# Kernel optimization log

Measured on AMD Instinct MI355X. Metric: run time of the kernel, lower is better.

Reference implementation:

```python
import jax, jax.numpy as jnp
import numpy as np
import math

NDIM = 1
K = 7            # kernel_size ** ndim
C = 256          # channels
G = C            # depthwise -> groups == channels
GC = 1           # group_channels
HID = 32
OMEGA = 30.0
OFFSET_SCALE = 2.0
MIN_SIGMA, MAX_SIGMA = 0.05, 0.5
INIT_SIGMA = 0.3


def setup_inputs() -> dict:
    key = jax.random.key(0)
    ks = jax.random.split(key, 24)
    B, L = 4, 4096
    init_raw = math.log(math.exp(INIT_SIGMA) - 1.0)
    nrm = jax.random.normal
    d = {
        "x": nrm(ks[0], (B, L, C), jnp.float32),
        "raw_sigma": jnp.full((NDIM,), init_raw, jnp.float32),
        # input/output projections (stored as (in, out): y = x @ W + b)
        "w_in": nrm(ks[1], (C, C)) * (1.0 / np.sqrt(C)),
        "b_in": nrm(ks[2], (C,)) * 0.01,
        "w_out": nrm(ks[3], (C, C)) * (1.0 / np.sqrt(C)),
        "b_out": nrm(ks[4], (C,)) * 0.01,
        # dw_conv: depthwise 3-tap conv (OIH with I=1), then 1x1 conv (in,out)
        "dw1_w": nrm(ks[5], (C, 1, 3)) * (1.0 / np.sqrt(3)),
        "dw1_b": nrm(ks[6], (C,)) * 0.01,
        "dw2_w": nrm(ks[7], (C, C)) * (1.0 / np.sqrt(C)),
        "dw2_b": nrm(ks[8], (C,)) * 0.01,
        # offset / mask nets (zero-init in original; small random to exercise sampling)
        "w_off": nrm(ks[9], (C, G * K * NDIM)) * 0.01,
        "b_off": nrm(ks[10], (G * K * NDIM,)) * 0.01,
        "w_mask": nrm(ks[11], (C, G * K)) * 0.01,
        "b_mask": nrm(ks[12], (G * K,)) * 0.01,
        # kernel net: Linear(1,32), SiLU, Linear(32,32), SiLU, Linear(32,32), SiLU, Linear(32, G*GC)
        "k0_w": nrm(ks[13], (NDIM, HID)) * 1.0,
        "k0_b": nrm(ks[14], (HID,)) * 0.01,
        "k1_w": nrm(ks[15], (HID, HID)) * (1.0 / np.sqrt(HID)),
        "k1_b": nrm(ks[16], (HID,)) * 0.01,
        "k2_w": nrm(ks[17], (HID, HID)) * (1.0 / np.sqrt(HID)),
        "k2_b": nrm(ks[18], (HID,)) * 0.01,
        "k3_w": nrm(ks[19], (HID, G * GC)) * (1.0 / np.sqrt(HID)),
        "k3_b": nrm(ks[20], (G * GC,)) * 0.01,
    }
    return d


def _forward(x, raw_sigma, w_in, b_in, w_out, b_out, dw1_w, dw1_b, dw2_w, dw2_b,
             w_off, b_off, w_mask, b_mask, k0_w, k0_b, k1_w, k1_b, k2_w, k2_b, k3_w, k3_b):
    B, L, Cc = x.shape
    grid = jnp.linspace(-0.5, 0.5, K)[:, None]                       # (K, NDIM)
    ref_off = (jnp.arange(K, dtype=x.dtype) - K // 2)[:, None]        # (K, NDIM)

    sigma = jnp.clip(jax.nn.softplus(raw_sigma), MIN_SIGMA, MAX_SIGMA)

    x_proj = x @ w_in + b_in                                          # (B, L, C)

    # dw_conv: depthwise conv3 -> SiLU -> conv1x1, on (B, C, L)
    xc = jnp.transpose(x, (0, 2, 1))
    h = jax.lax.conv_general_dilated(xc, dw1_w, (1,), ((1, 1),),
                                     dimension_numbers=("NCH", "OIH", "NCH"),
                                     feature_group_count=Cc)
    h = jax.nn.silu(h + dw1_b[None, :, None])
    h = jnp.einsum("bcl,cd->bdl", h, dw2_w) + dw2_b[None, :, None]
    x_dw = jnp.transpose(h, (0, 2, 1))                                # (B, L, C)

    # Gaussian envelope over kernel taps
    d2 = (grid / jnp.clip(sigma, 1e-6, None)[None, :]) ** 2
    env = jnp.exp(-0.5 * d2.sum(-1))                                  # (K,)
    env = env / jnp.maximum(env.sum(), 1e-8)

    # implicit kernel weights from kernel net (SIREN-style input scaling)
    kh = jax.nn.silu(grid * OMEGA @ k0_w + k0_b)
    kh = jax.nn.silu(kh @ k1_w + k1_b)
    kh = jax.nn.silu(kh @ k2_w + k2_b)
    kernel_weights = kh @ k3_w + k3_b                                 # (K, G*GC)

    offsets = jnp.tanh(x_dw @ w_off + b_off).reshape(B, L, G, K, NDIM) * OFFSET_SCALE
    pos = jnp.arange(L, dtype=x.dtype).reshape(1, L, 1, 1, 1)
    abs_pos = pos + ref_off.reshape(1, 1, 1, K, NDIM) + offsets       # (B,L,G,K,1)

    # ---- bilinear (linear, ndim=1) sampling with gather ----
    p = jnp.clip(abs_pos[..., 0], 0.0, L - 1)                         # (B,L,G,K)
    pf = p.astype(jnp.int32)
    pc = jnp.minimum(pf + 1, L - 1)
    wc = (p - pf.astype(p.dtype))[..., None]                          # (B,L,G,K,1)
    wf = 1.0 - wc

    x_t = x_proj.reshape(B, L, G, GC).transpose(0, 2, 1, 3)           # (B,G,L,GC)

    def gather(idx):  # idx (B,L,G,K) int -> (B,L,G,K,GC)
        it = idx.transpose(0, 2, 1, 3).reshape(B, G, L * K, 1)
        g = jnp.take_along_axis(x_t, it, axis=2)
        return g.reshape(B, G, L, K, GC).transpose(0, 2, 1, 3, 4)

    sampled = gather(pf) * wf + gather(pc) * wc                       # (B,L,G,K,GC)

    kw = kernel_weights.reshape(G, GC, K).transpose(0, 2, 1)          # (G,K,GC) (raw reshape as in original)
    sampled = sampled * kw[None, None]

    raw_mask = (x_dw @ w_mask + b_mask).reshape(B, L, G, K) * env.reshape(1, 1, 1, K)
    attn = jax.nn.softmax(raw_mask, axis=-1)

    out = (sampled * attn[..., None]).sum(3).reshape(B, L, Cc)
    out = out @ w_out + b_out

    offset_reg = (offsets ** 2).mean()
    entropy = -(attn * jnp.log(attn + 1e-8)).sum(-1).mean()
    return out, offset_reg, -entropy


def reference(x, raw_sigma, w_in, b_in, w_out, b_out, dw1_w, dw1_b, dw2_w, dw2_b,
              w_off, b_off, w_mask, b_mask, k0_w, k0_b, k1_w, k1_b, k2_w, k2_b, k3_w, k3_b):
    return _forward(x, raw_sigma, w_in, b_in, w_out, b_out, dw1_w, dw1_b, dw2_w, dw2_b,
                    w_off, b_off, w_mask, b_mask, k0_w, k0_b, k1_w, k1_b, k2_w, k2_b, k3_w, k3_b)
```

## Files before the change

kernel.cpp:

```cpp
#include <hip/hip_runtime.h>
#include <hip/hip_bf16.h>
#include <hip/hip_fp16.h>
#include <math.h>

#define BB   4
#define LL   4096
#define CCH  256
#define KK   7
#define HIDN 32
#define MTOT (BB * LL)
#define NOFF (CCH * KK)
#define NP   4096
#define NBLK ((NP / 128) * (MTOT / 128))

#define LOG2E  1.4426950408889634f
#define NLOG2E2 (-2.8853900817779268f)
#define LN2    0.6931471805599453f

typedef __attribute__((ext_vector_type(8))) short short8;
typedef __attribute__((ext_vector_type(4))) short short4v;
typedef __attribute__((ext_vector_type(4))) float f32x4;
typedef __attribute__((ext_vector_type(2))) __fp16 fp16x2;
typedef __attribute__((address_space(1))) void gvoid_t;
typedef __attribute__((address_space(3))) void svoid_t;

__device__ __forceinline__ float siluf(float v) { return v / (1.0f + expf(-v)); }
__device__ __forceinline__ float bf2f(ushort u) { unsigned x = (unsigned)u << 16; return __uint_as_float(x); }
__device__ __forceinline__ float h2f(ushort u) { __half_raw hr; hr.x = u; return __half2float(__half(hr)); }
__device__ __forceinline__ unsigned pkh(float a, float b) {
    union { fp16x2 h; unsigned u; } cv;
    cv.h = __builtin_amdgcn_cvt_pkrtz(a, b);
    return cv.u;
}

__global__ __launch_bounds__(256) void precompute_kernel(
    const float* __restrict__ raw_sigma,
    const float* __restrict__ k0w, const float* __restrict__ k0b,
    const float* __restrict__ k1w, const float* __restrict__ k1b,
    const float* __restrict__ k2w, const float* __restrict__ k2b,
    const float* __restrict__ k3w, const float* __restrict__ k3b,
    const float* __restrict__ b_off, const float* __restrict__ b_mask,
    float* __restrict__ kws2, float* __restrict__ bcomb,
    float* __restrict__ env)
{
    __shared__ float h0[KK][HIDN];
    __shared__ float h1[KK][HIDN];
    __shared__ float h2[KK][HIDN];
    __shared__ float flatw[NOFF];
    __shared__ float envs[KK];
    int t = threadIdx.x;
    if (t < KK * HIDN) {
        int k = t / HIDN, j = t % HIDN;
        float gk = -0.5f + (float)k * (1.0f / 6.0f);
        float v = gk * 30.0f * k0w[j] + k0b[j];
        h0[k][j] = siluf(v);
    }
    __syncthreads();
    if (t < KK * HIDN) {
        int k = t / HIDN, j = t % HIDN;
        float s = k1b[j];
        #pragma unroll
        for (int i = 0; i < HIDN; ++i) s += h0[k][i] * k1w[i * HIDN + j];
        h1[k][j] = siluf(s);
    }
    __syncthreads();
    if (t < KK * HIDN) {
        int k = t / HIDN, j = t % HIDN;
        float s = k2b[j];
        #pragma unroll
        for (int i = 0; i < HIDN; ++i) s += h1[k][i] * k2w[i * HIDN + j];
        h2[k][j] = siluf(s);
    }
    __syncthreads();
    for (int k = 0; k < KK; ++k) {
        float s = k3b[t];
        #pragma unroll
        for (int i = 0; i < HIDN; ++i) s += h2[k][i] * k3w[i * CCH + t];
        flatw[k * CCH + t] = s;
    }
    if (t == 0) {
        float sp = log1pf(expf(raw_sigma[0]));
        sp = fminf(fmaxf(sp, 0.05f), 0.5f);
        float sg = fmaxf(sp, 1e-6f);
        float ev[KK]; float ssum = 0.0f;
        for (int k = 0; k < KK; ++k) {
            float gk = -0.5f + (float)k * (1.0f / 6.0f);
            float d = gk / sg;
            ev[k] = expf(-0.5f * d * d);
            ssum += ev[k];
        }
        ssum = fmaxf(ssum, 1e-8f);
        for (int k = 0; k < KK; ++k) { env[k] = ev[k] / ssum; envs[k] = ev[k] / ssum; }
    }
    __syncthreads();
    #pragma unroll
    for (int k = 0; k < KK; ++k) kws2[t * 8 + k] = flatw[t * KK + k];
    kws2[t * 8 + 7] = 0.0f;
    #pragma unroll
    for (int k = 0; k < KK; ++k) {
        bcomb[t * 16 + k]     = b_off[t * KK + k] * NLOG2E2;
        bcomb[t * 16 + 8 + k] = b_mask[t * KK + k] * envs[k] * LOG2E;
    }
    bcomb[t * 16 + 7]  = 0.0f;
    bcomb[t * 16 + 15] = 0.0f;
}

__global__ __launch_bounds__(256) void prep_kernel(
    const float* __restrict__ w_in, const float* __restrict__ dw2_w,
    const float* __restrict__ w_out, const float* __restrict__ w_off,
    const float* __restrict__ w_mask, const float* __restrict__ env,
    __hip_bfloat16* __restrict__ wtin, __hip_bfloat16* __restrict__ wtdw2,
    __hip_bfloat16* __restrict__ wtout, __hip_bfloat16* __restrict__ wtcomb)
{
    const int task = blockIdx.y;
    const int tid = threadIdx.x;
    if (task == 5) {
        if (blockIdx.x >= 64) return;
        unsigned u = blockIdx.x * 256 + tid;
        unsigned row_sel = u >> 5, chunk = u & 31;
        unsigned g = row_sel >> 1, which = row_sel & 1;
        unsigned row = g * 16 + 7 + which * 8;
        short8 z = {};
        *(short8*)((ushort*)wtcomb + (size_t)row * 256 + chunk * 8) = z;
        return;
    }
    const float* src; __hip_bfloat16* dst; int N; int mode = 0;
    switch (task) {
        case 0: src = w_in;  dst = wtin;  N = 256;  break;
        case 1: src = dw2_w; dst = wtdw2; N = 256;  break;
        case 2: src = w_out; dst = wtout; N = 256;  break;
        case 3: src = w_off;  dst = wtcomb; N = NOFF; mode = 1; break;
        default: src = w_mask; dst = wtcomb; N = NOFF; mode = 2; break;
    }
    int ntiles = 4 * (N / 64);
    if (blockIdx.x >= (unsigned)ntiles) return;
    int tk = (blockIdx.x & 3) * 64;
    int tn = (blockIdx.x >> 2) * 64;
    __shared__ float t[64][65];
    #pragma unroll
    for (int i = 0; i < 16; ++i) {
        int e = i * 256 + tid, kk = e >> 6, nn = e & 63;
        t[kk][nn] = src[(size_t)(tk + kk) * N + tn + nn];
    }
    __syncthreads();
    #pragma unroll
    for (int i = 0; i < 16; ++i) {
        int e = i * 256 + tid, nn = e >> 6, kk = e & 63;
        int c = tn + nn;
        float v = t[kk][nn];
        int cp;
        if (mode == 0) cp = c;
        else {
            int g = c / KK, k = c % KK;
            if (mode == 1) { cp = g * 16 + k;     v *= NLOG2E2; }
            else           { cp = g * 16 + 8 + k; v *= env[k] * LOG2E; }
        }
        dst[(size_t)cp * 256 + tk + kk] = __float2bfloat16(v);
    }
}

__global__ __launch_bounds__(256) void dwconv_conv_kernel(
    const float* __restrict__ x, const float* __restrict__ w1,
    const float* __restrict__ b1, __hip_bfloat16* __restrict__ xbf,
    __hip_bfloat16* __restrict__ h)
{
    size_t base = ((size_t)blockIdx.x * 256 + threadIdx.x) * 4;
    int c = (int)(base & (CCH - 1));
    int l = (int)((base >> 8) & (LL - 1));
    float4 xm = *(const float4*)&x[base];
    float4 xl = make_float4(0.f, 0.f, 0.f, 0.f);
    float4 xr = make_float4(0.f, 0.f, 0.f, 0.f);
    if (l > 0)      xl = *(const float4*)&x[base - CCH];
    if (l < LL - 1) xr = *(const float4*)&x[base + CCH];
    float vm[4] = {xm.x, xm.y, xm.z, xm.w};
    float vl[4] = {xl.x, xl.y, xl.z, xl.w};
    float vr[4] = {xr.x, xr.y, xr.z, xr.w};
    ushort xo[4], ho[4];
    #pragma unroll
    for (int j = 0; j < 4; ++j) {
        int cc = c + j;
        float s = vm[j] * w1[cc * 3 + 1] + vl[j] * w1[cc * 3 + 0] + vr[j] * w1[cc * 3 + 2] + b1[cc];
        __hip_bfloat16 hb = __float2bfloat16(siluf(s));
        __hip_bfloat16 xb = __float2bfloat16(vm[j]);
        ho[j] = *(ushort*)&hb;
        xo[j] = *(ushort*)&xb;
    }
    *(short4v*)&xbf[base] = *(short4v*)xo;
    *(short4v*)&h[base]   = *(short4v*)ho;
}

template<int OUTBF>
__device__ __forceinline__ void gemm_core(
    const __hip_bfloat16* __restrict__ A, const __hip_bfloat16* __restrict__ Bt,
    const float* __restrict__ bias, void* __restrict__ C, int N, char* lds,
    int bx, int by)
{
    char* As = lds;
    char* Bs = lds + 16384;
    const int tid = threadIdx.x, lane = tid & 63, w = tid >> 6;
    const int wr = w >> 1, wc = w & 1;
    const size_t m0 = (size_t)by * 128, n0 = (size_t)bx * 128;

    const int srow = w * 32 + (lane >> 3);
    const int sgr  = (lane & 7) ^ ((lane >> 3) & 7);
    const __hip_bfloat16* a_src = A  + (m0 + srow) * 256 + sgr * 8;
    const __hip_bfloat16* b_src = Bt + (n0 + srow) * 256 + sgr * 8;
    char* a_dst = As + (w * 32) * 128;
    char* b_dst = Bs + (w * 32) * 128;

    f32x4 acc[4][4] = {};

    for (int kt = 0; kt < 4; ++kt) {
        const int k0 = kt * 64;
        #pragma unroll
        for (int inst = 0; inst < 4; ++inst) {
            __builtin_amdgcn_global_load_lds((gvoid_t*)(a_src + k0 + (size_t)inst * 8 * 256),
                                             (svoid_t*)(a_dst + inst * 1024), 16, 0, 0);
            __builtin_amdgcn_global_load_lds((gvoid_t*)(b_src + k0 + (size_t)inst * 8 * 256),
                                             (svoid_t*)(b_dst + inst * 1024), 16, 0, 0);
        }
        __syncthreads();
        #pragma unroll
        for (int ks = 0; ks < 2; ++ks) {
            short8 a[4], b[4];
            #pragma unroll
            for (int i = 0; i < 4; ++i) {
                int mr = wr * 64 + i * 16 + (lane & 15);
                int gk = ks * 4 + (lane >> 4);
                a[i] = *(const short8*)(As + mr * 128 + ((gk ^ (mr & 7)) << 4));
                int nr = wc * 64 + i * 16 + (lane & 15);
                b[i] = *(const short8*)(Bs + nr * 128 + ((gk ^ (nr & 7)) << 4));
            }
            #pragma unroll
            for (int i = 0; i < 4; ++i)
                #pragma unroll
                for (int j = 0; j < 4; ++j)
                    acc[i][j] = __builtin_amdgcn_mfma_f32_16x16x32_bf16(a[i], b[j], acc[i][j], 0, 0, 0);
        }
        __syncthreads();
    }
    #pragma unroll
    for (int j = 0; j < 4; ++j) {
        int col = (int)n0 + wc * 64 + j * 16 + (lane & 15);
        float bb = bias[col];
        #pragma unroll
        for (int i = 0; i < 4; ++i) {
            size_t row0 = m0 + wr * 64 + i * 16 + ((lane >> 4) << 2);
            f32x4 v = acc[i][j];
            #pragma unroll
            for (int q = 0; q < 4; ++q) {
                float val = v[q] + bb;
                if (OUTBF) ((__hip_bfloat16*)C)[(row0 + q) * N + col] = __float2bfloat16(val);
                else       ((float*)C)[(row0 + q) * N + col] = val;
            }
        }
    }
}

__global__ __launch_bounds__(256) void gemm_dual_k256(
    const __hip_bfloat16* __restrict__ A0, const __hip_bfloat16* __restrict__ Bt0,
    const float* __restrict__ bias0, __hip_bfloat16* __restrict__ C0,
    const __hip_bfloat16* __restrict__ A1, const __hip_bfloat16* __restrict__ Bt1,
    const float* __restrict__ bias1, __hip_bfloat16* __restrict__ C1)
{
    __shared__ __align__(16) char lds[32768];
    if (blockIdx.z == 0) gemm_core<1>(A0, Bt0, bias0, C0, 256, lds, blockIdx.x, blockIdx.y);
    else                 gemm_core<1>(A1, Bt1, bias1, C1, 256, lds, blockIdx.x, blockIdx.y);
}

__global__ __launch_bounds__(256) void gemm_out_k256(
    const __hip_bfloat16* __restrict__ A, const __hip_bfloat16* __restrict__ Bt,
    const float* __restrict__ bias, float* __restrict__ C)
{
    __shared__ __align__(16) char lds[32768];
    gemm_core<0>(A, Bt, bias, C, 256, lds, blockIdx.x, blockIdx.y);
}

__global__ __launch_bounds__(256) void gemm_fused_sample(
    const __hip_bfloat16* __restrict__ A,
    const __hip_bfloat16* __restrict__ Bt,
    const float* __restrict__ bcomb,
    const __hip_bfloat16* __restrict__ xproj,
    const float* __restrict__ kws2,
    __hip_bfloat16* __restrict__ out_pre,
    float* __restrict__ partials)
{
    __shared__ __align__(16) char lds[35072];
    char* As = lds;
    char* Bs = lds + 16384;
    const int tid = threadIdx.x, lane = tid & 63, w = tid >> 6;
    const int wr = w >> 1, wc = w & 1;
    const size_t m0 = (size_t)blockIdx.y * 128;
    const int n0 = blockIdx.x * 128, g0 = blockIdx.x * 8;
    const int l0 = (int)(m0 & (LL - 1));
    const int bidx = (int)(m0 >> 12);

    if (tid < 140) {
        int rr = min(max(l0 - 5 + tid, 0), LL - 1);
        const ushort* src = (const ushort*)xproj + ((size_t)bidx * LL + rr) * CCH + g0;
        __builtin_amdgcn_global_load_lds((gvoid_t*)src,
            (svoid_t*)(lds + 32768 + (tid >> 6) * 1024), 16, 0, 0);
    }

    const int srow = w * 32 + (lane >> 3);
    const int sgr  = (lane & 7) ^ ((lane >> 3) & 7);
    const __hip_bfloat16* a_src = A  + (m0 + srow) * 256 + sgr * 8;
    const __hip_bfloat16* b_src = Bt + (size_t)(n0 + srow) * 256 + sgr * 8;
    char* a_dst = As + (w * 32) * 128;
    char* b_dst = Bs + (w * 32) * 128;

    f32x4 acc[4][4] = {};

    for (int kt = 0; kt < 4; ++kt) {
        const int k0 = kt * 64;
        #pragma unroll
        for (int inst = 0; inst < 4; ++inst) {
            __builtin_amdgcn_global_load_lds((gvoid_t*)(a_src + k0 + (size_t)inst * 8 * 256),
                                             (svoid_t*)(a_dst + inst * 1024), 16, 0, 0);
            __builtin_amdgcn_global_load_lds((gvoid_t*)(b_src + k0 + (size_t)inst * 8 * 256),
                                             (svoid_t*)(b_dst + inst * 1024), 16, 0, 0);
        }
        __syncthreads();
        #pragma unroll
        for (int ks = 0; ks < 2; ++ks) {
            short8 a[4], b[4];
            #pragma unroll
            for (int i = 0; i < 4; ++i) {
                int mr = wr * 64 + i * 16 + (lane & 15);
                int gk = ks * 4 + (lane >> 4);
                a[i] = *(const short8*)(As + mr * 128 + ((gk ^ (mr & 7)) << 4));
                int nr = wc * 64 + i * 16 + (lane & 15);
                b[i] = *(const short8*)(Bs + nr * 128 + ((gk ^ (nr & 7)) << 4));
            }
            #pragma unroll
            for (int i = 0; i < 4; ++i)
                #pragma unroll
                for (int j = 0; j < 4; ++j)
                    acc[j][i] = __builtin_amdgcn_mfma_f32_16x16x32_bf16(b[j], a[i], acc[j][i], 0, 0, 0);
        }
        __syncthreads();
    }

    {
        const int rl = lane & 15, grp = lane >> 4;
        #pragma unroll
        for (int j = 0; j < 4; ++j) {
            float4 bi = *(const float4*)&bcomb[n0 + wc * 64 + j * 16 + grp * 4];
            const int gran = wc * 8 + j * 2 + (grp >> 1);
            #pragma unroll
            for (int i = 0; i < 4; ++i) {
                f32x4 v = acc[j][i];
                uint2 pk;
                pk.x = pkh(v[0] + bi.x, v[1] + bi.y);
                pk.y = pkh(v[2] + bi.z, v[3] + bi.w);
                int row = wr * 64 + i * 16 + rl;
                int addr = row * 256 + ((gran ^ rl) << 4) + (grp & 1) * 8;
                *(uint2*)(lds + addr) = pk;
            }
        }
    }
    __syncthreads();

    const ushort* XsL = (const ushort*)(lds + 32768);
    const int gg = tid & 7, rb = tid >> 3;
    float kwv[KK];
    {
        const float* kp = &kws2[(size_t)(g0 + gg) * 8];
        float4 ka = *(const float4*)kp;
        float4 kb = *(const float4*)(kp + 4);
        kwv[0] = ka.x; kwv[1] = ka.y; kwv[2] = ka.z; kwv[3] = ka.w;
        kwv[4] = kb.x; kwv[5] = kb.y; kwv[6] = kb.z;
    }
    float reg_acc = 0.0f, ent_acc = 0.0f;
    #pragma unroll
    for (int pp = 0; pp < 4; ++pp) {
        const int r = rb + 32 * pp;
        short8 ca = *(const short8*)(lds + r * 256 + (((2 * gg) ^ (r & 15)) << 4));
        short8 cb = *(const short8*)(lds + r * 256 + (((2 * gg + 1) ^ (r & 15)) << 4));
        float mv[KK];
        float mx = -1e30f;
        #pragma unroll
        for (int k = 0; k < KK; ++k) { mv[k] = h2f((ushort)cb[k]); mx = fmaxf(mx, mv[k]); }
        const int l = l0 + r;
        float es = 0.0f, tacc = 0.0f, o = 0.0f;
        #pragma unroll
        for (int k = 0; k < KK; ++k) {
            float d = mv[k] - mx;
            float e = exp2f(d);
            es += e; tacc += e * d;
            float zp = fminf(fmaxf(h2f((ushort)ca[k]), -80.f), 80.f);
            float ee = exp2f(zp);
            float ov = 2.0f * (1.0f - ee) / (1.0f + ee);
            reg_acc += ov * ov;
            float p = fminf(fmaxf((float)(l + k - 3) + ov, 0.0f), 4095.0f);
            int pf = (int)p;
            float wcf = p - (float)pf;
            int ix  = pf - (l0 - 5);
            int ixc = min(pf + 1, LL - 1) - (l0 - 5);
            float sv = bf2f(XsL[ix * 8 + gg]) * (1.0f - wcf) + bf2f(XsL[ixc * 8 + gg]) * wcf;
            o += sv * kwv[k] * e;
        }
        float inv = 1.0f / es;
        ent_acc += tacc * inv - __log2f(es);
        out_pre[(m0 + r) * CCH + g0 + gg] = __float2bfloat16(o * inv);
    }

    #pragma unroll
    for (int d = 1; d < 64; d <<= 1) {
        reg_acc += __shfl_xor(reg_acc, d);
        ent_acc += __shfl_xor(ent_acc, d);
    }
    __syncthreads();
    float* redv = (float*)lds;
    if (lane == 0) { redv[w] = reg_acc; redv[4 + w] = ent_acc; }
    __syncthreads();
    if (tid == 0) {
        float r2 = redv[0] + redv[1] + redv[2] + redv[3];
        float e2 = redv[4] + redv[5] + redv[6] + redv[7];
        int bid = blockIdx.y * gridDim.x + blockIdx.x;
        partials[bid * 2]     = r2;
        partials[bid * 2 + 1] = e2 * LN2;
    }
}

__global__ __launch_bounds__(256) void finalize_kernel(
    const float* __restrict__ partials, float* __restrict__ out_tail)
{
    __shared__ float redr[256], rede[256];
    int t = threadIdx.x;
    float r = 0.0f, e = 0.0f;
    for (int i = t; i < NBLK; i += 256) {
        r += partials[2 * i];
        e += partials[2 * i + 1];
    }
    redr[t] = r; rede[t] = e;
    __syncthreads();
    for (int s = 128; s > 0; s >>= 1) {
        if (t < s) { redr[t] += redr[t + s]; rede[t] += rede[t + s]; }
        __syncthreads();
    }
    if (t == 0) {
        out_tail[0] = redr[0] / 29360128.0f;
        out_tail[1] = rede[0] / 4194304.0f;
    }
}

extern "C" void kernel_launch(void* const* d_in, const int* in_sizes, int n_in,
                              void* d_out, int out_size, void* d_ws, size_t ws_size,
                              hipStream_t stream)
{
    const float* x         = (const float*)d_in[0];
    const float* raw_sigma = (const float*)d_in[1];
    const float* w_in      = (const float*)d_in[2];
    const float* b_in      = (const float*)d_in[3];
    const float* w_out     = (const float*)d_in[4];
    const float* b_out     = (const float*)d_in[5];
    const float* dw1_w     = (const float*)d_in[6];
    const float* dw1_b     = (const float*)d_in[7];
    const float* dw2_w     = (const float*)d_in[8];
    const float* dw2_b     = (const float*)d_in[9];
    const float* w_off     = (const float*)d_in[10];
    const float* b_off     = (const float*)d_in[11];
    const float* w_mask    = (const float*)d_in[12];
    const float* b_mask    = (const float*)d_in[13];
    const float* k0w       = (const float*)d_in[14];
    const float* k0b       = (const float*)d_in[15];
    const float* k1w       = (const float*)d_in[16];
    const float* k1b       = (const float*)d_in[17];
    const float* k2w       = (const float*)d_in[18];
    const float* k2b       = (const float*)d_in[19];
    const float* k3w       = (const float*)d_in[20];
    const float* k3b       = (const float*)d_in[21];

    char* ws = (char*)d_ws;
    const size_t MB8 = (size_t)8 * 1024 * 1024;
    __hip_bfloat16* xbf    = (__hip_bfloat16*)(ws + 0);
    __hip_bfloat16* hbf    = (__hip_bfloat16*)(ws + MB8);
    __hip_bfloat16* xdwbf  = (__hip_bfloat16*)(ws + 2 * MB8);
    __hip_bfloat16* xprojb = (__hip_bfloat16*)(ws + 3 * MB8);
    char* wbase = ws + 4 * MB8;
    __hip_bfloat16* wtin   = (__hip_bfloat16*)(wbase);
    __hip_bfloat16* wtdw2  = (__hip_bfloat16*)(wbase + 131072);
    __hip_bfloat16* wtout  = (__hip_bfloat16*)(wbase + 262144);
    __hip_bfloat16* wtcomb = (__hip_bfloat16*)(wbase + 393216);
    float* bcomb    = (float*)(wbase + 393216 + 2097152);
    float* kws2     = bcomb + NP;
    float* env      = kws2 + 2048;
    float* partials = env + 16;

    precompute_kernel<<<1, 256, 0, stream>>>(raw_sigma, k0w, k0b, k1w, k1b,
                                             k2w, k2b, k3w, k3b, b_off, b_mask,
                                             kws2, bcomb, env);
    prep_kernel<<<dim3(112, 6), 256, 0, stream>>>(w_in, dw2_w, w_out, w_off, w_mask, env,
                                                  wtin, wtdw2, wtout, wtcomb);
    dwconv_conv_kernel<<<(MTOT * CCH) / 1024, 256, 0, stream>>>(x, dw1_w, dw1_b, xbf, hbf);
    gemm_dual_k256<<<dim3(2, 128, 2), 256, 0, stream>>>(xbf, wtin, b_in, xprojb,
                                                        hbf, wtdw2, dw2_b, xdwbf);
    gemm_fused_sample<<<dim3(NP / 128, MTOT / 128), 256, 0, stream>>>(
        xdwbf, wtcomb, bcomb, xprojb, kws2, hbf, partials);
    gemm_out_k256<<<dim3(2, 128), 256, 0, stream>>>(hbf, wtout, b_out, (float*)d_out);
    finalize_kernel<<<1, 256, 0, stream>>>(partials, (float*)d_out + (size_t)MTOT * CCH);
}
```

Measured before the change: 150.2 us.

## Enlarge fused sample GEMM tile to 256 rows with 512-thread blocks

The fused offset/mask GEMM plus sampling kernel now runs each block over 256 M-rows with 8 waves instead of 128 rows with 4. The B (weight) tile is loaded cooperatively and shared across twice as many rows, which halves weight reloads per output. The halo of x_proj rows grows accordingly. The epilogue spills the accumulator to LDS in two 128-row halves, with extra barriers, to fit the larger tile. This raises LDS use to about 52KB per block and halves the grid, which may lower occupancy and add latency.

```diff
diff --git a/kernel.cpp b/kernel.cpp
--- a/kernel.cpp
+++ b/kernel.cpp
@@ -11,7 +11,8 @@
 #define MTOT (BB * LL)
 #define NOFF (CCH * KK)
 #define NP   4096
-#define NBLK ((NP / 128) * (MTOT / 128))
+#define NBLK ((NP / 128) * (MTOT / 256))
+#define XS_OFF 49152
 
 #define LOG2E  1.4426950408889634f
 #define NLOG2E2 (-2.8853900817779268f)
@@ -276,7 +277,7 @@
     gemm_core<0>(A, Bt, bias, C, 256, lds, blockIdx.x, blockIdx.y);
 }
 
-__global__ __launch_bounds__(256) void gemm_fused_sample(
+__global__ __launch_bounds__(512) void gemm_fused_sample(
     const __hip_bfloat16* __restrict__ A,
     const __hip_bfloat16* __restrict__ Bt,
     const float* __restrict__ bcomb,
@@ -285,41 +286,39 @@
     __hip_bfloat16* __restrict__ out_pre,
     float* __restrict__ partials)
 {
-    __shared__ __align__(16) char lds[35072];
-    char* As = lds;
-    char* Bs = lds + 16384;
+    __shared__ __align__(16) char lds[53504];
     const int tid = threadIdx.x, lane = tid & 63, w = tid >> 6;
     const int wr = w >> 1, wc = w & 1;
-    const size_t m0 = (size_t)blockIdx.y * 128;
+    const size_t m0 = (size_t)blockIdx.y * 256;
     const int n0 = blockIdx.x * 128, g0 = blockIdx.x * 8;
     const int l0 = (int)(m0 & (LL - 1));
     const int bidx = (int)(m0 >> 12);
 
-    if (tid < 140) {
+    if (tid < 267) {
         int rr = min(max(l0 - 5 + tid, 0), LL - 1);
         const ushort* src = (const ushort*)xproj + ((size_t)bidx * LL + rr) * CCH + g0;
         __builtin_amdgcn_global_load_lds((gvoid_t*)src,
-            (svoid_t*)(lds + 32768 + (tid >> 6) * 1024), 16, 0, 0);
-    }
-
-    const int srow = w * 32 + (lane >> 3);
-    const int sgr  = (lane & 7) ^ ((lane >> 3) & 7);
-    const __hip_bfloat16* a_src = A  + (m0 + srow) * 256 + sgr * 8;
-    const __hip_bfloat16* b_src = Bt + (size_t)(n0 + srow) * 256 + sgr * 8;
-    char* a_dst = As + (w * 32) * 128;
-    char* b_dst = Bs + (w * 32) * 128;
+            (svoid_t*)(lds + XS_OFF + (tid >> 6) * 1024), 16, 0, 0);
+    }
+
+    const int sgr = (lane & 7) ^ ((lane >> 3) & 7);
+    const __hip_bfloat16* a_src = A  + (m0 + w * 32 + (lane >> 3)) * 256 + sgr * 8;
+    const __hip_bfloat16* b_src = Bt + (size_t)(n0 + w * 16 + (lane >> 3)) * 256 + sgr * 8;
+    char* a_dst = lds + (w * 32) * 128;
+    char* b_dst = lds + 32768 + (w * 16) * 128;
 
     f32x4 acc[4][4] = {};
 
     for (int kt = 0; kt < 4; ++kt) {
         const int k0 = kt * 64;
         #pragma unroll
-        for (int inst = 0; inst < 4; ++inst) {
+        for (int inst = 0; inst < 4; ++inst)
             __builtin_amdgcn_global_load_lds((gvoid_t*)(a_src + k0 + (size_t)inst * 8 * 256),
                                              (svoid_t*)(a_dst + inst * 1024), 16, 0, 0);
+        #pragma unroll
+        for (int inst = 0; inst < 2; ++inst)
             __builtin_amdgcn_global_load_lds((gvoid_t*)(b_src + k0 + (size_t)inst * 8 * 256),
                                              (svoid_t*)(b_dst + inst * 1024), 16, 0, 0);
-        }
         __syncthreads();
         #pragma unroll
         for (int ks = 0; ks < 2; ++ks) {
@@ -328,9 +327,9 @@
             for (int i = 0; i < 4; ++i) {
                 int mr = wr * 64 + i * 16 + (lane & 15);
                 int gk = ks * 4 + (lane >> 4);
-                a[i] = *(const short8*)(As + mr * 128 + ((gk ^ (mr & 7)) << 4));
+                a[i] = *(const short8*)(lds + mr * 128 + ((gk ^ (mr & 7)) << 4));
                 int nr = wc * 64 + i * 16 + (lane & 15);
-                b[i] = *(const short8*)(Bs + nr * 128 + ((gk ^ (nr & 7)) << 4));
+                b[i] = *(const short8*)(lds + 32768 + nr * 128 + ((gk ^ (nr & 7)) << 4));
             }
             #pragma unroll
             for (int i = 0; i < 4; ++i)
@@ -341,27 +340,7 @@
         __syncthreads();
     }
 
-    {
-        const int rl = lane & 15, grp = lane >> 4;
-        #pragma unroll
-        for (int j = 0; j < 4; ++j) {
-            float4 bi = *(const float4*)&bcomb[n0 + wc * 64 + j * 16 + grp * 4];
-            const int gran = wc * 8 + j * 2 + (grp >> 1);
-            #pragma unroll
-            for (int i = 0; i < 4; ++i) {
-                f32x4 v = acc[j][i];
-                uint2 pk;
-                pk.x = pkh(v[0] + bi.x, v[1] + bi.y);
-                pk.y = pkh(v[2] + bi.z, v[3] + bi.w);
-                int row = wr * 64 + i * 16 + rl;
-                int addr = row * 256 + ((gran ^ rl) << 4) + (grp & 1) * 8;
-                *(uint2*)(lds + addr) = pk;
-            }
-        }
-    }
-    __syncthreads();
-
-    const ushort* XsL = (const ushort*)(lds + 32768);
+    const ushort* XsL = (const ushort*)(lds + XS_OFF);
     const int gg = tid & 7, rb = tid >> 3;
     float kwv[KK];
     {
@@ -372,37 +351,62 @@
         kwv[4] = kb.x; kwv[5] = kb.y; kwv[6] = kb.z;
     }
     float reg_acc = 0.0f, ent_acc = 0.0f;
-    #pragma unroll
-    for (int pp = 0; pp < 4; ++pp) {
-        const int r = rb + 32 * pp;
-        short8 ca = *(const short8*)(lds + r * 256 + (((2 * gg) ^ (r & 15)) << 4));
-        short8 cb = *(const short8*)(lds + r * 256 + (((2 * gg + 1) ^ (r & 15)) << 4));
-        float mv[KK];
-        float mx = -1e30f;
-        #pragma unroll
-        for (int k = 0; k < KK; ++k) { mv[k] = h2f((ushort)cb[k]); mx = fmaxf(mx, mv[k]); }
-        const int l = l0 + r;
-        float es = 0.0f, tacc = 0.0f, o = 0.0f;
-        #pragma unroll
-        for (int k = 0; k < KK; ++k) {
-            float d = mv[k] - mx;
-            float e = exp2f(d);
-            es += e; tacc += e * d;
-            float zp = fminf(fmaxf(h2f((ushort)ca[k]), -80.f), 80.f);
-            float ee = exp2f(zp);
-            float ov = 2.0f * (1.0f - ee) / (1.0f + ee);
-            reg_acc += ov * ov;
-            float p = fminf(fmaxf((float)(l + k - 3) + ov, 0.0f), 4095.0f);
-            int pf = (int)p;
-            float wcf = p - (float)pf;
-            int ix  = pf - (l0 - 5);
-            int ixc = min(pf + 1, LL - 1) - (l0 - 5);
-            float sv = bf2f(XsL[ix * 8 + gg]) * (1.0f - wcf) + bf2f(XsL[ixc * 8 + gg]) * wcf;
-            o += sv * kwv[k] * e;
-        }
-        float inv = 1.0f / es;
-        ent_acc += tacc * inv - __log2f(es);
-        out_pre[(m0 + r) * CCH + g0 + gg] = __float2bfloat16(o * inv);
+
+    #pragma unroll
+    for (int c = 0; c < 2; ++c) {
+        if ((w >> 2) == c) {
+            const int rl = lane & 15, grp = lane >> 4;
+            #pragma unroll
+            for (int j = 0; j < 4; ++j) {
+                float4 bi = *(const float4*)&bcomb[n0 + wc * 64 + j * 16 + grp * 4];
+                const int gran = wc * 8 + j * 2 + (grp >> 1);
+                #pragma unroll
+                for (int i = 0; i < 4; ++i) {
+                    f32x4 v = acc[j][i];
+                    uint2 pk;
+                    pk.x = pkh(v[0] + bi.x, v[1] + bi.y);
+                    pk.y = pkh(v[2] + bi.z, v[3] + bi.w);
+                    int row_local = (wr & 1) * 64 + i * 16 + rl;
+                    int addr = row_local * 256 + ((gran ^ rl) << 4) + (grp & 1) * 8;
+                    *(uint2*)(lds + addr) = pk;
+                }
+            }
+        }
+        __syncthreads();
+
+        #pragma unroll
+        for (int pp = 0; pp < 2; ++pp) {
+            const int rloc = rb + 64 * pp;
+            short8 ca = *(const short8*)(lds + rloc * 256 + (((2 * gg) ^ (rloc & 15)) << 4));
+            short8 cb = *(const short8*)(lds + rloc * 256 + (((2 * gg + 1) ^ (rloc & 15)) << 4));
+            float mv[KK];
+            float mx = -1e30f;
+            #pragma unroll
+            for (int k = 0; k < KK; ++k) { mv[k] = h2f((ushort)cb[k]); mx = fmaxf(mx, mv[k]); }
+            const int l = l0 + c * 128 + rloc;
+            float es = 0.0f, tacc = 0.0f, o = 0.0f;
+            #pragma unroll
+            for (int k = 0; k < KK; ++k) {
+                float d = mv[k] - mx;
+                float e = exp2f(d);
+                es += e; tacc += e * d;
+                float zp = fminf(fmaxf(h2f((ushort)ca[k]), -80.f), 80.f);
+                float ee = exp2f(zp);
+                float ov = 2.0f * (1.0f - ee) / (1.0f + ee);
+                reg_acc += ov * ov;
+                float p = fminf(fmaxf((float)(l + k - 3) + ov, 0.0f), 4095.0f);
+                int pf = (int)p;
+                float wcf = p - (float)pf;
+                int ix  = pf - (l0 - 5);
+                int ixc = min(pf + 1, LL - 1) - (l0 - 5);
+                float sv = bf2f(XsL[ix * 8 + gg]) * (1.0f - wcf) + bf2f(XsL[ixc * 8 + gg]) * wcf;
+                o += sv * kwv[k] * e;
+            }
+            float inv = 1.0f / es;
+            ent_acc += tacc * inv - __log2f(es);
+            out_pre[(m0 + c * 128 + rloc) * CCH + g0 + gg] = __float2bfloat16(o * inv);
+        }
+        __syncthreads();
     }
 
     #pragma unroll
@@ -410,13 +414,13 @@
         reg_acc += __shfl_xor(reg_acc, d);
         ent_acc += __shfl_xor(ent_acc, d);
     }
-    __syncthreads();
     float* redv = (float*)lds;
-    if (lane == 0) { redv[w] = reg_acc; redv[4 + w] = ent_acc; }
+    if (lane == 0) { redv[w] = reg_acc; redv[8 + w] = ent_acc; }
     __syncthreads();
     if (tid == 0) {
-        float r2 = redv[0] + redv[1] + redv[2] + redv[3];
-        float e2 = redv[4] + redv[5] + redv[6] + redv[7];
+        float r2 = 0.0f, e2 = 0.0f;
+        #pragma unroll
+        for (int i = 0; i < 8; ++i) { r2 += redv[i]; e2 += redv[8 + i]; }
         int bid = blockIdx.y * gridDim.x + blockIdx.x;
         partials[bid * 2]     = r2;
         partials[bid * 2 + 1] = e2 * LN2;
@@ -496,7 +500,7 @@
     dwconv_conv_kernel<<<(MTOT * CCH) / 1024, 256, 0, stream>>>(x, dw1_w, dw1_b, xbf, hbf);
     gemm_dual_k256<<<dim3(2, 128, 2), 256, 0, stream>>>(xbf, wtin, b_in, xprojb,
                                                         hbf, wtdw2, dw2_b, xdwbf);
-    gemm_fused_sample<<<dim3(NP / 128, MTOT / 128), 256, 0, stream>>>(
+    gemm_fused_sample<<<dim3(NP / 128, MTOT / 256), 512, 0, stream>>>(
         xdwbf, wtcomb, bcomb, xprojb, kws2, hbf, partials);
     gemm_out_k256<<<dim3(2, 128), 256, 0, stream>>>(hbf, wtout, b_out, (float*)d_out);
     finalize_kernel<<<1, 256, 0, stream>>>(partials, (float*)d_out + (size_t)MTOT * CCH);
```

Measured after the change: 174.7 us. 1.16x slower.
